# Optimization experiments

Measured on AMD Instinct MI355X. Metric: run time of the kernel, lower is better.

Reference implementation:

```python
import jax, jax.numpy as jnp
import numpy as np

N_HEADS = 16
HEAD_DIM = 64
ROPE_THETA = 10000.0


def rotate_half(x):
    x1, x2 = jnp.split(x, 2, axis=-1)
    return jnp.concatenate([-x2, x1], axis=-1)


def setup_inputs() -> dict:
    key = jax.random.key(0)
    k0, k1, k2 = jax.random.split(key, 3)
    B, L, C = 2, 2048, 1024
    x = jax.random.normal(k0, (B, L, C), dtype=jnp.float32)
    # causal additive bias, as used by VAR-style blockwise masks (here full causal)
    causal = jnp.tril(jnp.ones((L, L), dtype=bool))
    attn_bias = jnp.where(causal, 0.0, -1e9).astype(jnp.float32)[None, None]
    position_ids = jnp.broadcast_to(jnp.arange(L, dtype=jnp.int32), (B, L))
    qkv_w = 0.02 * jax.random.normal(k1, (3 * C, C), dtype=jnp.float32)
    q_bias = jnp.zeros((C,), jnp.float32)
    v_bias = jnp.zeros((C,), jnp.float32)
    proj_w = 0.02 * jax.random.normal(k2, (C, C), dtype=jnp.float32)
    proj_b = jnp.zeros((C,), jnp.float32)
    return {"x": x, "attn_bias": attn_bias, "position_ids": position_ids,
            "qkv_w": qkv_w, "q_bias": q_bias, "v_bias": v_bias,
            "proj_w": proj_w, "proj_b": proj_b}


def reference(x, attn_bias, position_ids, qkv_w, q_bias, v_bias, proj_w, proj_b):
    B, L, C = x.shape
    H, D = N_HEADS, HEAD_DIM
    # fused QKV projection with concatenated (q_bias, 0, v_bias)
    bias = jnp.concatenate([q_bias, jnp.zeros_like(q_bias), v_bias])
    qkv = (jnp.einsum('blc,oc->blo', x, qkv_w) + bias).reshape(B, L, 3, H, D)
    q = jnp.transpose(qkv[:, :, 0], (0, 2, 1, 3))  # [B,H,L,D]
    k = jnp.transpose(qkv[:, :, 1], (0, 2, 1, 3))
    v = jnp.transpose(qkv[:, :, 2], (0, 2, 1, 3))
    # Llama rotary embedding: cos/sin [B,L,D] -> unsqueeze dim=1
    inv_freq = 1.0 / (ROPE_THETA ** (jnp.arange(0, D, 2, dtype=jnp.float32) / D))
    freqs = position_ids.astype(jnp.float32)[:, :, None] * inv_freq  # [B,L,D/2]
    emb = jnp.concatenate([freqs, freqs], axis=-1)
    cos = jnp.cos(emb)[:, None]  # [B,1,L,D]
    sin = jnp.sin(emb)[:, None]
    q = q * cos + rotate_half(q) * sin
    k = k * cos + rotate_half(k) * sin
    # slow_attn: (q*scale) @ k^T + bias -> softmax -> @ v
    scale = 0.25 / np.sqrt(D).astype(np.float32)
    attn = jnp.einsum('bhqd,bhkd->bhqk', q * scale, k) + attn_bias
    attn = jax.nn.softmax(attn, axis=-1)
    out = jnp.einsum('bhqk,bhkd->bhqd', attn, v)
    out = out.transpose(0, 2, 1, 3).reshape(B, L, C)
    return jnp.einsum('blc,oc->blo', out, proj_w) + proj_b
```

## Files before the change

kernel.cpp:

```cpp
#include <hip/hip_runtime.h>

typedef unsigned short u16;
typedef unsigned int u32;
typedef __attribute__((ext_vector_type(8))) short short8;
typedef __attribute__((ext_vector_type(4))) float f32x4;
typedef __attribute__((ext_vector_type(2))) unsigned int u32x2;
typedef __attribute__((ext_vector_type(4))) unsigned short u16x4;
typedef __attribute__((ext_vector_type(8))) unsigned short u16x8;

#define AS1 __attribute__((address_space(1)))
#define AS3 __attribute__((address_space(3)))

__device__ __forceinline__ u16 f2bf(float f) {
  u32 u = __builtin_bit_cast(u32, f);
  u32 r = u + 0x7FFFu + ((u >> 16) & 1u);
  return (u16)(r >> 16);
}
__device__ __forceinline__ float bf2f(u16 h) {
  u32 u = ((u32)h) << 16;
  return __builtin_bit_cast(float, u);
}
__device__ __forceinline__ void gload_lds16(const void* g, void* l) {
  __builtin_amdgcn_global_load_lds((AS1 void*)g, (AS3 void*)l, 16, 0, 0);
}
__device__ __forceinline__ float fexp2(float x) {
  float r;
  asm("v_exp_f32 %0, %1" : "=v"(r) : "v"(x));
  return r;
}

#define QSCALE 0.04508422002778011f

__device__ __forceinline__ void cvt_body(const float* __restrict__ src, u16* __restrict__ dst,
                                         int i) {
  float4 v = ((const float4*)src)[i];
  u16x4 o;
  o[0] = f2bf(v.x); o[1] = f2bf(v.y); o[2] = f2bf(v.z); o[3] = f2bf(v.w);
  ((u16x4*)dst)[i] = o;
}

__global__ __launch_bounds__(256)
void pre_kernel(const float* __restrict__ x, const float* __restrict__ w1,
                const float* __restrict__ w2, const int* __restrict__ pos,
                u16* __restrict__ x_bf, u16* __restrict__ w1_bf, u16* __restrict__ w2_bf,
                float* __restrict__ tab) {
  int bid = blockIdx.x;
  int t = threadIdx.x;
  if (bid < 4096) {
    cvt_body(x, x_bf, bid * 256 + t);
  } else if (bid < 7168) {
    cvt_body(w1, w1_bf, (bid - 4096) * 256 + t);
  } else if (bid < 8192) {
    cvt_body(w2, w2_bf, (bid - 7168) * 256 + t);
  } else {
    int idx = (bid - 8192) * 256 + t;
    int i = idx & 31;
    int bl = idx >> 5;
    float p = (float)pos[bl];
    float inv_freq = 1.0f / powf(10000.0f, (2.0f * (float)i) / 64.0f);
    float ang = p * inv_freq;
    tab[(size_t)bl * 64 + i] = cosf(ang);
    tab[(size_t)bl * 64 + 32 + i] = sinf(ang);
  }
}

template <bool OUT_BF16>
__global__ __launch_bounds__(256)
void gemm_bt_kernel(const u16* __restrict__ A, const u16* __restrict__ Bw,
                    void* __restrict__ Cout, const float* __restrict__ bias,
                    int M, int N, int K, int NXT) {
  __shared__ alignas(16) u16 As[128 * 64];
  __shared__ alignas(16) u16 Bs[128 * 64];
  const int tid = threadIdx.x;
  const int lane = tid & 63, wave = tid >> 6;
  const int wr = wave >> 1, wc = wave & 1;
  const int nblk = gridDim.x;
  const int lin = (blockIdx.x & 7) * (nblk >> 3) + (blockIdx.x >> 3);
  const int m0 = (lin / NXT) * 128, n0 = (lin % NXT) * 128;
  const int r = lane & 15, g = lane >> 4;

  f32x4 acc[4][4] = {};

  const int nk = K >> 6;
  for (int kt = 0; kt < nk; ++kt) {
    const int k0 = kt << 6;
#pragma unroll
    for (int c = 0; c < 4; ++c) {
      int i = c * 256 + tid;
      int row = i >> 3, slot = i & 7;
      int ss = slot ^ (row & 7);
      const u16* gA = A + (size_t)(m0 + row) * K + k0 + ss * 8;
      const u16* gB = Bw + (size_t)(n0 + row) * K + k0 + ss * 8;
      void* lA = (char*)As + c * 4096 + wave * 1024;
      void* lB = (char*)Bs + c * 4096 + wave * 1024;
      gload_lds16(gA, lA);
      gload_lds16(gB, lB);
    }
    __syncthreads();
#pragma unroll
    for (int kk = 0; kk < 2; ++kk) {
      short8 af[4], bf[4];
#pragma unroll
      for (int m = 0; m < 4; ++m) {
        int row = wr * 64 + m * 16 + r;
        int byte = row * 128 + (((kk * 4 + g) ^ (row & 7)) << 4);
        af[m] = *(const short8*)((const char*)As + byte);
      }
#pragma unroll
      for (int n = 0; n < 4; ++n) {
        int row = wc * 64 + n * 16 + r;
        int byte = row * 128 + (((kk * 4 + g) ^ (row & 7)) << 4);
        bf[n] = *(const short8*)((const char*)Bs + byte);
      }
#pragma unroll
      for (int m = 0; m < 4; ++m)
#pragma unroll
        for (int n = 0; n < 4; ++n)
          acc[m][n] = __builtin_amdgcn_mfma_f32_16x16x32_bf16(af[m], bf[n], acc[m][n], 0, 0, 0);
    }
    __syncthreads();
  }

  if constexpr (OUT_BF16) {
    u16* C = (u16*)Cout;
#pragma unroll
    for (int m = 0; m < 4; ++m) {
      int rg = m0 + wr * 64 + m * 16 + g * 4;
#pragma unroll
      for (int n = 0; n < 4; ++n) {
        int cg = n0 + wc * 64 + n * 16 + r;
#pragma unroll
        for (int j = 0; j < 4; ++j)
          C[(size_t)(rg + j) * N + cg] = f2bf(acc[m][n][j]);
      }
    }
  } else {
    float* C = (float*)Cout;
#pragma unroll
    for (int m = 0; m < 4; ++m) {
      int rg = m0 + wr * 64 + m * 16 + g * 4;
#pragma unroll
      for (int n = 0; n < 4; ++n) {
        int cg = n0 + wc * 64 + n * 16 + r;
        float bv = bias[cg];
#pragma unroll
        for (int j = 0; j < 4; ++j)
          C[(size_t)(rg + j) * N + cg] = acc[m][n][j] + bv;
      }
    }
  }
}

__global__ __launch_bounds__(256)
void gemm_bt64_kernel(const u16* __restrict__ A, const u16* __restrict__ Bw,
                      float* __restrict__ Cout, const float* __restrict__ bias,
                      int M, int N, int K, int NXT) {
  __shared__ alignas(16) u16 As[128 * 64];
  __shared__ alignas(16) u16 Bs[64 * 64];
  const int tid = threadIdx.x;
  const int lane = tid & 63, wave = tid >> 6;
  const int wr = wave >> 1, wc = wave & 1;
  const int nblk = gridDim.x;
  const int lin = (blockIdx.x & 7) * (nblk >> 3) + (blockIdx.x >> 3);
  const int m0 = (lin / NXT) * 128, n0 = (lin % NXT) * 64;
  const int r = lane & 15, g = lane >> 4;

  f32x4 acc[4][2] = {};

  const int nk = K >> 6;
  for (int kt = 0; kt < nk; ++kt) {
    const int k0 = kt << 6;
#pragma unroll
    for (int c = 0; c < 4; ++c) {
      int i = c * 256 + tid;
      int row = i >> 3, slot = i & 7;
      int ss = slot ^ (row & 7);
      const u16* gA = A + (size_t)(m0 + row) * K + k0 + ss * 8;
      void* lA = (char*)As + c * 4096 + wave * 1024;
      gload_lds16(gA, lA);
    }
#pragma unroll
    for (int c = 0; c < 2; ++c) {
      int i = c * 256 + tid;
      int row = i >> 3, slot = i & 7;
      int ss = slot ^ (row & 7);
      const u16* gB = Bw + (size_t)(n0 + row) * K + k0 + ss * 8;
      void* lB = (char*)Bs + c * 4096 + wave * 1024;
      gload_lds16(gB, lB);
    }
    __syncthreads();
#pragma unroll
    for (int kk = 0; kk < 2; ++kk) {
      short8 af[4], bf[2];
#pragma unroll
      for (int m = 0; m < 4; ++m) {
        int row = wr * 64 + m * 16 + r;
        int byte = row * 128 + (((kk * 4 + g) ^ (row & 7)) << 4);
        af[m] = *(const short8*)((const char*)As + byte);
      }
#pragma unroll
      for (int n = 0; n < 2; ++n) {
        int row = wc * 32 + n * 16 + r;
        int byte = row * 128 + (((kk * 4 + g) ^ (row & 7)) << 4);
        bf[n] = *(const short8*)((const char*)Bs + byte);
      }
#pragma unroll
      for (int m = 0; m < 4; ++m)
#pragma unroll
        for (int n = 0; n < 2; ++n)
          acc[m][n] = __builtin_amdgcn_mfma_f32_16x16x32_bf16(af[m], bf[n], acc[m][n], 0, 0, 0);
    }
    __syncthreads();
  }

#pragma unroll
  for (int m = 0; m < 4; ++m) {
    int rg = m0 + wr * 64 + m * 16 + g * 4;
#pragma unroll
    for (int n = 0; n < 2; ++n) {
      int cg = n0 + wc * 32 + n * 16 + r;
      float bv = bias[cg];
#pragma unroll
      for (int j = 0; j < 4; ++j)
        Cout[(size_t)(rg + j) * N + cg] = acc[m][n][j] + bv;
    }
  }
}

__global__ __launch_bounds__(256)
void mid_kernel(const u16* __restrict__ qkv, const float* __restrict__ tab,
                const float* __restrict__ q_bias, const float* __restrict__ v_bias,
                u16* __restrict__ Qo, u16* __restrict__ Ko, u16* __restrict__ vt) {
  __shared__ alignas(16) u16 tile[64][72];
  int bid = blockIdx.x;
  int t = threadIdx.x;
  if (bid < 4096) {
    int bl = bid;
    int b = bl >> 11, l = bl & 2047;
    const float* tr = tab + (size_t)bl * 64;
    const u16* base = qkv + (size_t)bl * 3072;
#pragma unroll
    for (int pp = 0; pp < 2; ++pp) {
      int p = t + pp * 256;
      int h = p >> 5, d = p & 31;
      float c = tr[d], s = tr[32 + d];
      size_t o = ((size_t)(b * 16 + h) * 2048 + l) * 64 + d;
      float x1 = bf2f(base[h * 64 + d]) + q_bias[h * 64 + d];
      float x2 = bf2f(base[h * 64 + d + 32]) + q_bias[h * 64 + d + 32];
      Qo[o]      = f2bf((x1 * c - x2 * s) * QSCALE);
      Qo[o + 32] = f2bf((x2 * c + x1 * s) * QSCALE);
      x1 = bf2f(base[1024 + h * 64 + d]);
      x2 = bf2f(base[1024 + h * 64 + d + 32]);
      Ko[o]      = f2bf(x1 * c - x2 * s);
      Ko[o + 32] = f2bf(x2 * c + x1 * s);
    }
  } else {
    int bid2 = bid - 4096;
    int bh = bid2 >> 5;
    int b = bh >> 4, h = bh & 15;
    int l0 = (bid2 & 31) * 64;
    int rr = t >> 2;
    int c0 = (t & 3) * 16;
    const u16* src = qkv + ((size_t)(b * 2048 + l0 + rr)) * 3072 + 2048 + h * 64 + c0;
    u16x8 a = *(const u16x8*)src;
    u16x8 bb = *(const u16x8*)(src + 8);
#pragma unroll
    for (int i = 0; i < 8; ++i) {
      a[i]  = f2bf(bf2f(a[i])  + v_bias[h * 64 + c0 + i]);
      bb[i] = f2bf(bf2f(bb[i]) + v_bias[h * 64 + c0 + 8 + i]);
    }
    *(u16x8*)&tile[rr][c0] = a;
    *(u16x8*)&tile[rr][c0 + 8] = bb;
    __syncthreads();
    int d = t >> 2;
    int lc = (t & 3) * 16;
    u16x8 o1, o2;
#pragma unroll
    for (int i = 0; i < 8; ++i) {
      o1[i] = tile[lc + i][d];
      o2[i] = tile[lc + 8 + i][d];
    }
    u16* dst = vt + ((size_t)bh * 64 + d) * 2048 + l0 + lc;
    *(u16x8*)dst = o1;
    *(u16x8*)(dst + 8) = o2;
  }
}

__global__ __launch_bounds__(512)
void attn_kernel(const u16* __restrict__ Q, const u16* __restrict__ Kmat,
                 const u16* __restrict__ Vt, u16* __restrict__ O) {
  __shared__ alignas(16) u16 Ks[3][64 * 64];
  __shared__ alignas(16) u16 Vs[3][64 * 64];
  __shared__ alignas(16) u16 Pbuf[8][1024];
  const int tid = threadIdx.x;
  const int lane = tid & 63;
  const int wave = tid >> 6;
  const int id = blockIdx.x;
  const int xcd = id & 7, rank = id >> 3;
  const int bh = xcd + 8 * (rank & 3);
  const int xqA = 31 - (rank >> 2);
  const int wt = wave >> 2;
  const int xq = wt ? (xqA - 16) : xqA;
  const int ntA = xqA + 1;
  const int nt = xq + 1;
  const int b = bh >> 4, h = bh & 15;
  const int r = lane & 15, g = lane >> 4;

  const u16* Kb = Kmat + (size_t)bh * 2048 * 64;
  const u16* Vb = Vt + (size_t)bh * 64 * 2048;

  const int srow = wave * 8 + (lane >> 3);
  const int sslot = (lane & 7) ^ (srow & 7);

#define STAGE(tt, bb) do { \
    gload_lds16(Kb + ((size_t)((tt) * 64 + srow)) * 64 + sslot * 8, \
                (char*)Ks[bb] + wave * 1024); \
    gload_lds16(Vb + (size_t)srow * 2048 + (tt) * 64 + sslot * 8, \
                (char*)Vs[bb] + wave * 1024); \
  } while (0)

  u16* Pw = Pbuf[wave];
  const int qrow0 = xq * 64 + (wave & 3) * 16;
  const u16* Qb = Q + ((size_t)bh * 2048 + qrow0) * 64;

  short8 qf[2];
#pragma unroll
  for (int kk = 0; kk < 2; ++kk)
    qf[kk] = *(const short8*)(Qb + r * 64 + kk * 32 + g * 8);

  short8 ones;
#pragma unroll
  for (int i = 0; i < 8; ++i) ones[i] = (short)0x3F80;

  f32x4 o_acc[4] = {};
  f32x4 l_acc = {};

  STAGE(0, 0);
  STAGE(1, 1);
  asm volatile("s_waitcnt vmcnt(2)" ::: "memory");
  __builtin_amdgcn_s_barrier();

  for (int t = 0; t < ntA; ++t) {
    if (t + 2 < ntA) STAGE(t + 2, (t + 2) % 3);

    if (t < nt) {
      const char* Kc = (const char*)Ks[t % 3];
      const char* Vc = (const char*)Vs[t % 3];
      const int kv0 = t * 64;

      f32x4 s[4] = {};
      __builtin_amdgcn_s_setprio(1);
#pragma unroll
      for (int ct = 0; ct < 4; ++ct) {
#pragma unroll
        for (int kk = 0; kk < 2; ++kk) {
          int row = ct * 16 + r;
          int byte = row * 128 + (((kk * 4 + g) ^ (row & 7)) << 4);
          short8 kf = *(const short8*)(Kc + byte);
          s[ct] = __builtin_amdgcn_mfma_f32_16x16x32_bf16(kf, qf[kk], s[ct], 0, 0, 0);
        }
      }
      __builtin_amdgcn_s_setprio(0);

      if (kv0 + 63 > qrow0) {
        int qrow = qrow0 + r;
#pragma unroll
        for (int ct = 0; ct < 4; ++ct)
#pragma unroll
          for (int j = 0; j < 4; ++j) {
            int kv = kv0 + ct * 16 + 4 * g + j;
            if (kv > qrow) s[ct][j] = -1e30f;
          }
      }

      u32x2 pk[4];
#pragma unroll
      for (int ct = 0; ct < 4; ++ct) {
        float p0 = fexp2(s[ct][0]);
        float p1 = fexp2(s[ct][1]);
        float p2 = fexp2(s[ct][2]);
        float p3 = fexp2(s[ct][3]);
        u32 lo, hi;
        asm("v_cvt_pk_bf16_f32 %0, %1, %2" : "=v"(lo) : "v"(p0), "v"(p1));
        asm("v_cvt_pk_bf16_f32 %0, %1, %2" : "=v"(hi) : "v"(p2), "v"(p3));
        pk[ct][0] = lo;
        pk[ct][1] = hi;
      }

#pragma unroll
      for (int ct = 0; ct < 4; ++ct) {
        int byte = r * 128 + ((32 * ct + 8 * g) ^ ((r & 7) << 4));
        *(u32x2*)((char*)Pw + byte) = pk[ct];
      }

      __builtin_amdgcn_s_setprio(1);
#pragma unroll
      for (int kk = 0; kk < 2; ++kk) {
        int byte = r * 128 + (((kk * 4 + g) ^ (r & 7)) << 4);
        short8 pf = *(const short8*)((const char*)Pw + byte);
        l_acc = __builtin_amdgcn_mfma_f32_16x16x32_bf16(pf, ones, l_acc, 0, 0, 0);
#pragma unroll
        for (int n = 0; n < 4; ++n) {
          int row = n * 16 + r;
          int vbyte = row * 128 + (((kk * 4 + g) ^ (row & 7)) << 4);
          short8 vf = *(const short8*)(Vc + vbyte);
          o_acc[n] = __builtin_amdgcn_mfma_f32_16x16x32_bf16(pf, vf, o_acc[n], 0, 0, 0);
        }
      }
      __builtin_amdgcn_s_setprio(0);
    }

    if (t + 1 < ntA) {
      if (t + 2 < ntA) {
        asm volatile("s_waitcnt vmcnt(2)" ::: "memory");
      } else {
        asm volatile("s_waitcnt vmcnt(0)" ::: "memory");
      }
      __builtin_amdgcn_s_barrier();
    }
  }
#undef STAGE

  float ij[4];
#pragma unroll
  for (int j = 0; j < 4; ++j) ij[j] = 1.0f / l_acc[j];
#pragma unroll
  for (int n = 0; n < 4; ++n)
#pragma unroll
    for (int j = 0; j < 4; ++j) {
      size_t idx = ((size_t)b * 2048 + qrow0 + 4 * g + j) * 1024 + h * 64 + n * 16 + r;
      O[idx] = f2bf(o_acc[n][j] * ij[j]);
    }
}

extern "C" void kernel_launch(void* const* d_in, const int* in_sizes, int n_in,
                              void* d_out, int out_size, void* d_ws, size_t ws_size,
                              hipStream_t stream) {
  const float* x      = (const float*)d_in[0];
  const int*   pos    = (const int*)d_in[2];
  const float* qkv_w  = (const float*)d_in[3];
  const float* q_bias = (const float*)d_in[4];
  const float* v_bias = (const float*)d_in[5];
  const float* proj_w = (const float*)d_in[6];
  const float* proj_b = (const float*)d_in[7];
  float* out = (float*)d_out;

  char* ws = (char*)d_ws;
  u16* x_bf    = (u16*)(ws + 0);
  u16* w1_bf   = (u16*)(ws + 8388608);
  u16* w2_bf   = (u16*)(ws + 14680064);
  u16* qkv_bf  = (u16*)(ws + 16777216);
  u16* q_bf    = (u16*)(ws + 41943040);
  u16* k_bf    = (u16*)(ws + 50331648);
  u16* vt_bf   = (u16*)(ws + 58720256);
  u16* attn_bf = (u16*)(ws + 67108864);
  float* tab   = (float*)(ws + 75497472);

  pre_kernel<<<8704, 256, 0, stream>>>(x, qkv_w, proj_w, pos, x_bf, w1_bf, w2_bf, tab);
  gemm_bt_kernel<true><<<768, 256, 0, stream>>>(x_bf, w1_bf, qkv_bf, nullptr,
                                                4096, 3072, 1024, 24);
  mid_kernel<<<5120, 256, 0, stream>>>(qkv_bf, tab, q_bias, v_bias, q_bf, k_bf, vt_bf);
  attn_kernel<<<512, 512, 0, stream>>>(q_bf, k_bf, vt_bf, attn_bf);
  gemm_bt64_kernel<<<512, 256, 0, stream>>>(attn_bf, w2_bf, out, proj_b,
                                            4096, 1024, 1024, 16);
}
```

Measured before the change: 112.9 us.

## Load V fragments directly from global into registers instead of LDS staging

Removes the triple-buffered V tiles from shared memory in the attention kernel. Each wave now loads its V MFMA operands straight from global memory into registers at the start of each KV iteration, so they can overlap with the QK^T and softmax work. The wait counts are adjusted since only K is staged asynchronously. This frees LDS and removes the LDS reads of V, but every wave now fetches the same V tile from global or L2, multiplying V read traffic and exposing global load latency.

```diff
diff --git a/kernel.cpp b/kernel.cpp
--- a/kernel.cpp
+++ b/kernel.cpp
@@ -290,7 +290,6 @@
 void attn_kernel(const u16* __restrict__ Q, const u16* __restrict__ Kmat,
                  const u16* __restrict__ Vt, u16* __restrict__ O) {
   __shared__ alignas(16) u16 Ks[3][64 * 64];
-  __shared__ alignas(16) u16 Vs[3][64 * 64];
   __shared__ alignas(16) u16 Pbuf[8][1024];
   const int tid = threadIdx.x;
   const int lane = tid & 63;
@@ -312,12 +311,9 @@
   const int srow = wave * 8 + (lane >> 3);
   const int sslot = (lane & 7) ^ (srow & 7);
 
-#define STAGE(tt, bb) do { \
+#define STAGE(tt, bb) \
     gload_lds16(Kb + ((size_t)((tt) * 64 + srow)) * 64 + sslot * 8, \
-                (char*)Ks[bb] + wave * 1024); \
-    gload_lds16(Vb + (size_t)srow * 2048 + (tt) * 64 + sslot * 8, \
-                (char*)Vs[bb] + wave * 1024); \
-  } while (0)
+                (char*)Ks[bb] + wave * 1024)
 
   u16* Pw = Pbuf[wave];
   const int qrow0 = xq * 64 + (wave & 3) * 16;
@@ -337,16 +333,27 @@
 
   STAGE(0, 0);
   STAGE(1, 1);
-  asm volatile("s_waitcnt vmcnt(2)" ::: "memory");
+  asm volatile("s_waitcnt vmcnt(1)" ::: "memory");
   __builtin_amdgcn_s_barrier();
 
   for (int t = 0; t < ntA; ++t) {
+    const int kv0 = t * 64;
+
+    short8 vf[2][4];
+    if (t < nt) {
+#pragma unroll
+      for (int kk = 0; kk < 2; ++kk)
+#pragma unroll
+        for (int n = 0; n < 4; ++n)
+          vf[kk][n] = *(const short8*)(Vb + (size_t)(n * 16 + r) * 2048
+                                       + kv0 + kk * 32 + g * 8);
+      __builtin_amdgcn_sched_barrier(0);
+    }
+
     if (t + 2 < ntA) STAGE(t + 2, (t + 2) % 3);
 
     if (t < nt) {
       const char* Kc = (const char*)Ks[t % 3];
-      const char* Vc = (const char*)Vs[t % 3];
-      const int kv0 = t * 64;
 
       f32x4 s[4] = {};
       __builtin_amdgcn_s_setprio(1);
@@ -400,24 +407,20 @@
         short8 pf = *(const short8*)((const char*)Pw + byte);
         l_acc = __builtin_amdgcn_mfma_f32_16x16x32_bf16(pf, ones, l_acc, 0, 0, 0);
 #pragma unroll
-        for (int n = 0; n < 4; ++n) {
-          int row = n * 16 + r;
-          int vbyte = row * 128 + (((kk * 4 + g) ^ (row & 7)) << 4);
-          short8 vf = *(const short8*)(Vc + vbyte);
-          o_acc[n] = __builtin_amdgcn_mfma_f32_16x16x32_bf16(pf, vf, o_acc[n], 0, 0, 0);
-        }
+        for (int n = 0; n < 4; ++n)
+          o_acc[n] = __builtin_amdgcn_mfma_f32_16x16x32_bf16(pf, vf[kk][n],
+                                                            o_acc[n], 0, 0, 0);
       }
       __builtin_amdgcn_s_setprio(0);
-    }
-
-    if (t + 1 < ntA) {
+    } else {
       if (t + 2 < ntA) {
-        asm volatile("s_waitcnt vmcnt(2)" ::: "memory");
+        asm volatile("s_waitcnt vmcnt(1)" ::: "memory");
       } else {
         asm volatile("s_waitcnt vmcnt(0)" ::: "memory");
       }
-      __builtin_amdgcn_s_barrier();
-    }
+    }
+
+    if (t + 1 < ntA) __builtin_amdgcn_s_barrier();
   }
 #undef STAGE
 
```

After: 156.2 us. +38.3%, slower.

## Process two KV tiles per iteration with double-pair LDS buffering

Applied to the files above, without the earlier changes.

Restructures the attention main loop to handle two 64-wide KV tiles per iteration, with four K/V LDS buffers arranged as two ping-pong pairs. Both QK^T MFMA groups are issued back to back before the exp/softmax and PV stages, and there is now one barrier per tile pair. The aim is to halve barrier and waitcnt overhead and give the scheduler more independent MFMA work to interleave with exp. In exchange it uses more LDS and registers, which may lower occupancy, and it waits with vmcnt(0) instead of keeping a load in flight across the barrier.

```diff
diff --git a/kernel.cpp b/kernel.cpp
--- a/kernel.cpp
+++ b/kernel.cpp
@@ -289,8 +289,8 @@
 __global__ __launch_bounds__(512)
 void attn_kernel(const u16* __restrict__ Q, const u16* __restrict__ Kmat,
                  const u16* __restrict__ Vt, u16* __restrict__ O) {
-  __shared__ alignas(16) u16 Ks[3][64 * 64];
-  __shared__ alignas(16) u16 Vs[3][64 * 64];
+  __shared__ alignas(16) u16 Ks[4][64 * 64];
+  __shared__ alignas(16) u16 Vs[4][64 * 64];
   __shared__ alignas(16) u16 Pbuf[8][1024];
   const int tid = threadIdx.x;
   const int lane = tid & 63;
@@ -337,62 +337,101 @@
 
   STAGE(0, 0);
   STAGE(1, 1);
-  asm volatile("s_waitcnt vmcnt(2)" ::: "memory");
+  asm volatile("s_waitcnt vmcnt(0)" ::: "memory");
   __builtin_amdgcn_s_barrier();
 
-  for (int t = 0; t < ntA; ++t) {
-    if (t + 2 < ntA) STAGE(t + 2, (t + 2) % 3);
-
-    if (t < nt) {
-      const char* Kc = (const char*)Ks[t % 3];
-      const char* Vc = (const char*)Vs[t % 3];
-      const int kv0 = t * 64;
-
-      f32x4 s[4] = {};
-      __builtin_amdgcn_s_setprio(1);
-#pragma unroll
-      for (int ct = 0; ct < 4; ++ct) {
+  const int nss = (ntA + 1) >> 1;
+  for (int ss = 0; ss < nss; ++ss) {
+    const int t0 = 2 * ss, t1 = t0 + 1;
+    const int cb = 2 * (ss & 1);
+    const int sb = 2 * ((ss + 1) & 1);
+
+    if (t0 + 2 < ntA) STAGE(t0 + 2, sb);
+    if (t0 + 3 < ntA) STAGE(t0 + 3, sb + 1);
+
+    const bool a0 = (t0 < nt);
+    const bool a1 = (t1 < nt);
+
+    f32x4 s0[4] = {}, s1[4] = {};
+    __builtin_amdgcn_s_setprio(1);
+    if (a0) {
+      const char* Kc = (const char*)Ks[cb];
+#pragma unroll
+      for (int ct = 0; ct < 4; ++ct)
 #pragma unroll
         for (int kk = 0; kk < 2; ++kk) {
           int row = ct * 16 + r;
           int byte = row * 128 + (((kk * 4 + g) ^ (row & 7)) << 4);
           short8 kf = *(const short8*)(Kc + byte);
-          s[ct] = __builtin_amdgcn_mfma_f32_16x16x32_bf16(kf, qf[kk], s[ct], 0, 0, 0);
+          s0[ct] = __builtin_amdgcn_mfma_f32_16x16x32_bf16(kf, qf[kk], s0[ct], 0, 0, 0);
         }
-      }
-      __builtin_amdgcn_s_setprio(0);
-
-      if (kv0 + 63 > qrow0) {
-        int qrow = qrow0 + r;
-#pragma unroll
-        for (int ct = 0; ct < 4; ++ct)
-#pragma unroll
-          for (int j = 0; j < 4; ++j) {
-            int kv = kv0 + ct * 16 + 4 * g + j;
-            if (kv > qrow) s[ct][j] = -1e30f;
-          }
-      }
-
-      u32x2 pk[4];
+    }
+    if (a1) {
+      const char* Kc = (const char*)Ks[cb + 1];
+#pragma unroll
+      for (int ct = 0; ct < 4; ++ct)
+#pragma unroll
+        for (int kk = 0; kk < 2; ++kk) {
+          int row = ct * 16 + r;
+          int byte = row * 128 + (((kk * 4 + g) ^ (row & 7)) << 4);
+          short8 kf = *(const short8*)(Kc + byte);
+          s1[ct] = __builtin_amdgcn_mfma_f32_16x16x32_bf16(kf, qf[kk], s1[ct], 0, 0, 0);
+        }
+    }
+    __builtin_amdgcn_s_setprio(0);
+
+    if (a0 && t0 * 64 + 63 > qrow0) {
+      int qrow = qrow0 + r;
+#pragma unroll
+      for (int ct = 0; ct < 4; ++ct)
+#pragma unroll
+        for (int j = 0; j < 4; ++j) {
+          int kv = t0 * 64 + ct * 16 + 4 * g + j;
+          if (kv > qrow) s0[ct][j] = -1e30f;
+        }
+    }
+    if (a1 && t1 * 64 + 63 > qrow0) {
+      int qrow = qrow0 + r;
+#pragma unroll
+      for (int ct = 0; ct < 4; ++ct)
+#pragma unroll
+        for (int j = 0; j < 4; ++j) {
+          int kv = t1 * 64 + ct * 16 + 4 * g + j;
+          if (kv > qrow) s1[ct][j] = -1e30f;
+        }
+    }
+
+    u32x2 pk0[4], pk1[4];
+    if (a0) {
 #pragma unroll
       for (int ct = 0; ct < 4; ++ct) {
-        float p0 = fexp2(s[ct][0]);
-        float p1 = fexp2(s[ct][1]);
-        float p2 = fexp2(s[ct][2]);
-        float p3 = fexp2(s[ct][3]);
-        u32 lo, hi;
-        asm("v_cvt_pk_bf16_f32 %0, %1, %2" : "=v"(lo) : "v"(p0), "v"(p1));
-        asm("v_cvt_pk_bf16_f32 %0, %1, %2" : "=v"(hi) : "v"(p2), "v"(p3));
-        pk[ct][0] = lo;
-        pk[ct][1] = hi;
-      }
-
+        float p0 = fexp2(s0[ct][0]);
+        float p1 = fexp2(s0[ct][1]);
+        float p2 = fexp2(s0[ct][2]);
+        float p3 = fexp2(s0[ct][3]);
+        asm("v_cvt_pk_bf16_f32 %0, %1, %2" : "=v"(pk0[ct][0]) : "v"(p0), "v"(p1));
+        asm("v_cvt_pk_bf16_f32 %0, %1, %2" : "=v"(pk0[ct][1]) : "v"(p2), "v"(p3));
+      }
+    }
+    if (a1) {
+#pragma unroll
+      for (int ct = 0; ct < 4; ++ct) {
+        float p0 = fexp2(s1[ct][0]);
+        float p1 = fexp2(s1[ct][1]);
+        float p2 = fexp2(s1[ct][2]);
+        float p3 = fexp2(s1[ct][3]);
+        asm("v_cvt_pk_bf16_f32 %0, %1, %2" : "=v"(pk1[ct][0]) : "v"(p0), "v"(p1));
+        asm("v_cvt_pk_bf16_f32 %0, %1, %2" : "=v"(pk1[ct][1]) : "v"(p2), "v"(p3));
+      }
+    }
+
+    if (a0) {
 #pragma unroll
       for (int ct = 0; ct < 4; ++ct) {
         int byte = r * 128 + ((32 * ct + 8 * g) ^ ((r & 7) << 4));
-        *(u32x2*)((char*)Pw + byte) = pk[ct];
-      }
-
+        *(u32x2*)((char*)Pw + byte) = pk0[ct];
+      }
+      const char* Vc = (const char*)Vs[cb];
       __builtin_amdgcn_s_setprio(1);
 #pragma unroll
       for (int kk = 0; kk < 2; ++kk) {
@@ -410,12 +449,32 @@
       __builtin_amdgcn_s_setprio(0);
     }
 
-    if (t + 1 < ntA) {
-      if (t + 2 < ntA) {
-        asm volatile("s_waitcnt vmcnt(2)" ::: "memory");
-      } else {
-        asm volatile("s_waitcnt vmcnt(0)" ::: "memory");
-      }
+    if (a1) {
+#pragma unroll
+      for (int ct = 0; ct < 4; ++ct) {
+        int byte = r * 128 + ((32 * ct + 8 * g) ^ ((r & 7) << 4));
+        *(u32x2*)((char*)Pw + byte) = pk1[ct];
+      }
+      const char* Vc = (const char*)Vs[cb + 1];
+      __builtin_amdgcn_s_setprio(1);
+#pragma unroll
+      for (int kk = 0; kk < 2; ++kk) {
+        int byte = r * 128 + (((kk * 4 + g) ^ (r & 7)) << 4);
+        short8 pf = *(const short8*)((const char*)Pw + byte);
+        l_acc = __builtin_amdgcn_mfma_f32_16x16x32_bf16(pf, ones, l_acc, 0, 0, 0);
+#pragma unroll
+        for (int n = 0; n < 4; ++n) {
+          int row = n * 16 + r;
+          int vbyte = row * 128 + (((kk * 4 + g) ^ (row & 7)) << 4);
+          short8 vf = *(const short8*)(Vc + vbyte);
+          o_acc[n] = __builtin_amdgcn_mfma_f32_16x16x32_bf16(pf, vf, o_acc[n], 0, 0, 0);
+        }
+      }
+      __builtin_amdgcn_s_setprio(0);
+    }
+
+    if (ss + 1 < nss) {
+      asm volatile("s_waitcnt vmcnt(0)" ::: "memory");
       __builtin_amdgcn_s_barrier();
     }
   }
```

Result: faster. 110.3 us (-2.3%).
